# Kernel optimization log

Hardware: AMD Instinct MI355X
Metric: run time of the kernel (lower is better)

The kernel has to match this reference:

```python
import jax, jax.numpy as jnp
import numpy as np
import math

N_PTS = 262144
STEP_LENGTH = math.sqrt(3.0) / 1024.0  # step_length = sqrt(3)/steps


def pos_enc(x):
    # classic NeRF frequency encoding: identity + sin/cos at 10 octaves -> 3 + 3*2*10 = 63
    freqs = 2.0 ** jnp.arange(10, dtype=x.dtype)            # [10]
    xb = x[..., :, None] * freqs                            # [N,3,10]
    xb = xb.reshape(x.shape[0], -1)                         # [N,30]
    return jnp.concatenate([x, jnp.sin(xb), jnp.cos(xb)], axis=-1)  # [N,63]


def dir_enc(u):
    # 26-dim frequency encoding of (dir+1)/2 (color head input 283 = 256 + 26 + 1).
    # 13 sin/cos pairs: per-channel octaves 2^0..2^4, truncated to 13 frequencies.
    freqs = 2.0 ** jnp.arange(5, dtype=u.dtype)             # [5]
    z = (u[..., :, None] * freqs).reshape(u.shape[0], -1)[:, :13]  # [N,13]
    return jnp.concatenate([jnp.sin(z), jnp.cos(z)], axis=-1)      # [N,26]


def linear(x, w, b):
    return x @ w.T + b


def setup_inputs() -> dict:
    key = jax.random.key(0)
    ks = jax.random.split(key, 16)
    s = 0.05
    inp = {
        "position": jax.random.uniform(ks[0], (N_PTS, 3), dtype=jnp.float32),
        "direction": jax.random.uniform(ks[1], (N_PTS, 3), dtype=jnp.float32, minval=-1.0, maxval=1.0),
        "w1_in": jax.random.normal(ks[2], (256, 63), jnp.float32) * s,
        "b1_in": jnp.zeros((256,), jnp.float32),
        "w1_h": jax.random.normal(ks[3], (3, 256, 256), jnp.float32) * s,
        "b1_h": jnp.zeros((3, 256), jnp.float32),
        "w2_in": jax.random.normal(ks[4], (256, 319), jnp.float32) * s,
        "b2_in": jnp.zeros((256,), jnp.float32),
        "w2_h": jax.random.normal(ks[5], (3, 256, 256), jnp.float32) * s,
        "b2_h": jnp.zeros((3, 256), jnp.float32),
        # sigma head Linear(256,1)
        "w_sigma": jax.random.normal(ks[6], (1, 256), jnp.float32) * s,
        "b_sigma": jnp.zeros((1,), jnp.float32),
        # color head Linear(283,128) -> ReLU -> Linear(128,3)
        "w_c1": jax.random.normal(ks[7], (128, 283), jnp.float32) * s,
        "b_c1": jnp.zeros((128,), jnp.float32),
        "w_c2": jax.random.normal(ks[8], (3, 128), jnp.float32) * s,
        "b_c2": jnp.zeros((3,), jnp.float32),
    }
    return inp


def reference(position, direction,
              w1_in, b1_in, w1_h, b1_h,
              w2_in, b2_in, w2_h, b2_h,
              w_sigma, b_sigma, w_c1, b_c1, w_c2, b_c2):
    pe = pos_enc(position)                                  # [N,63]
    h = jax.nn.relu(linear(pe, w1_in, b1_in))               # [N,256]
    for i in range(3):
        h = jax.nn.relu(linear(h, w1_h[i], b1_h[i]))
    g = jax.nn.relu(linear(jnp.concatenate([h, pe], axis=-1), w2_in, b2_in))  # [N,256]
    for i in range(3):
        g = jax.nn.relu(linear(g, w2_h[i], b2_h[i]))
    sigma_raw = linear(g, w_sigma, b_sigma)                 # [N,1]
    # get_alpha: 1 - exp(-relu(sigma) * step_length)
    alphas = 1.0 - jnp.exp(-jax.nn.relu(sigma_raw) * STEP_LENGTH)             # [N,1]
    # get_rgb: shares base features; concat [256 | 26 | 1] = 283
    de = dir_enc((direction + 1.0) * 0.5)                   # [N,26]
    feats = jnp.concatenate([g, de, sigma_raw], axis=-1)    # [N,283]
    rgb = jax.nn.sigmoid(linear(jax.nn.relu(linear(feats, w_c1, b_c1)), w_c2, b_c2))  # [N,3]
    return (rgb, alphas)
```

## Files before the change

### kernel.cpp

```cpp
#include <hip/hip_runtime.h>
#include <hip/hip_bf16.h>

#define N_PTS 262144
#define STEP_LEN 0.0016914558667664818f

using f32x4 = __attribute__((ext_vector_type(4))) float;
using s8 = __attribute__((ext_vector_type(8))) short;

__device__ __forceinline__ float bf2f(short s) {
    union { unsigned int u; float f; } v;
    v.u = ((unsigned int)(unsigned short)s) << 16;
    return v.f;
}
__device__ __forceinline__ short f2bf(float f) {
    __hip_bfloat16 h = __float2bfloat16(f);
    return *reinterpret_cast<short*>(&h);
}

#define OFF_W1    0
#define OFF_L1H0  16384
#define OFF_L1H1  81920
#define OFF_L1H2  147456
#define OFF_W2    212992
#define OFF_L2H0  294912
#define OFF_L2H1  360448
#define OFF_L2H2  425984
#define OFF_C1G   491520
#define OFF_C1DE  524288
#define OFF_WSIG  528384
#define OFF_WC2   528640
#define WS_ELEMS  529024

__device__ __forceinline__ float hid_val(const float* __restrict__ W, int e) {
    int j = e & 7, lane = (e >> 3) & 63, nt = (e >> 9) & 15, ks = e >> 13;
    int n = nt * 16 + (lane & 15), hi = lane >> 4;
    int f = ks * 32 + ((j >> 2) << 4) + hi * 4 + (j & 3);
    return W[n * 256 + f];
}

__global__ void prep_weights(const float* __restrict__ w1_in,
                             const float* __restrict__ w1_h,
                             const float* __restrict__ w2_in,
                             const float* __restrict__ w2_h,
                             const float* __restrict__ w_c1,
                             const float* __restrict__ w_sigma,
                             const float* __restrict__ w_c2,
                             __hip_bfloat16* __restrict__ ws) {
    int i = blockIdx.x * blockDim.x + threadIdx.x;
    if (i >= WS_ELEMS) return;
    float v;
    if (i < OFF_L1H0) {
        int e = i;
        int j = e & 7, lane = (e >> 3) & 63, nt = (e >> 9) & 15, ks = e >> 13;
        int n = nt * 16 + (lane & 15), hi = lane >> 4;
        int f = ks * 32 + hi * 8 + j;
        v = (f < 63) ? w1_in[n * 63 + f] : 0.f;
    } else if (i < OFF_W2) {
        int e = i - OFF_L1H0; int sub = e >> 16; e &= 65535;
        v = hid_val(w1_h + sub * 65536, e);
    } else if (i < OFF_L2H0) {
        int e = i - OFF_W2;
        int j = e & 7, lane = (e >> 3) & 63, nt = (e >> 9) & 15, ks = e >> 13;
        int n = nt * 16 + (lane & 15), hi = lane >> 4;
        if (ks < 8) {
            int f = ks * 32 + ((j >> 2) << 4) + hi * 4 + (j & 3);
            v = w2_in[n * 319 + f];
        } else {
            int pf = (ks - 8) * 32 + hi * 8 + j;
            v = (pf < 63) ? w2_in[n * 319 + 256 + pf] : 0.f;
        }
    } else if (i < OFF_C1G) {
        int e = i - OFF_L2H0; int sub = e >> 16; e &= 65535;
        v = hid_val(w2_h + sub * 65536, e);
    } else if (i < OFF_C1DE) {
        int e = i - OFF_C1G;
        int j = e & 7, lane = (e >> 3) & 63, nt = (e >> 9) & 7, ks = e >> 12;
        int n = nt * 16 + (lane & 15), hi = lane >> 4;
        int f = ks * 32 + ((j >> 2) << 4) + hi * 4 + (j & 3);
        v = w_c1[n * 283 + f];
    } else if (i < OFF_WSIG) {
        int e = i - OFF_C1DE;
        int j = e & 7, lane = (e >> 3) & 63, nt = (e >> 9) & 7;
        int n = nt * 16 + (lane & 15), hi = lane >> 4;
        int k = 256 + hi * 8 + j;
        v = (k < 283) ? w_c1[n * 283 + k] : 0.f;
    } else if (i < OFF_WC2) {
        int e = i - OFF_WSIG;
        int j = e & 7, hi = (e >> 3) & 3, ks = e >> 5;
        int f = ks * 32 + ((j >> 2) << 4) + hi * 4 + (j & 3);
        v = w_sigma[f];
    } else {
        int e = i - OFF_WC2;
        int j = e & 7, hi = (e >> 3) & 3, ks = (e >> 5) & 3, ch = e >> 7;
        int f = ks * 32 + ((j >> 2) << 4) + hi * 4 + (j & 3);
        v = w_c2[ch * 128 + f];
    }
    ws[i] = __float2bfloat16(v);
}

__device__ __forceinline__ float enc3(int f, float x0, float x1, float x2) {
    if (f < 3) return (f == 0) ? x0 : ((f == 1) ? x1 : x2);
    if (f < 33) {
        int q = f - 3; int c = q / 10, o = q % 10;
        float xc = (c == 0) ? x0 : ((c == 1) ? x1 : x2);
        return __sinf(xc * (float)(1 << o));
    }
    if (f < 63) {
        int q = f - 33; int c = q / 10, o = q % 10;
        float xc = (c == 0) ? x0 : ((c == 1) ? x1 : x2);
        return __cosf(xc * (float)(1 << o));
    }
    return 0.f;
}

#define MFMA16 __builtin_amdgcn_mfma_f32_16x16x32_bf16

#define CHUNK1(WB, KSL, FA, FB) do { \
    _Pragma("unroll") \
    for (int nt = 0; nt < 16; ++nt) { \
        const s8 w = *(const s8*)((WB) + (((KSL)*16 + nt)*64 + lane)*16); \
        acc[nt][0] = MFMA16(w, (FA), acc[nt][0], 0, 0, 0); \
        acc[nt][1] = MFMA16(w, (FB), acc[nt][1], 0, 0, 0); \
    } } while (0)

#define CHUNK2(WB, KB) do { \
    _Pragma("unroll") \
    for (int ksl = 0; ksl < 2; ++ksl) { \
        _Pragma("unroll") \
        for (int nt = 0; nt < 16; ++nt) { \
            const s8 w = *(const s8*)((WB) + ((ksl*16 + nt)*64 + lane)*16); \
            acc[nt][0] = MFMA16(w, actA[(KB) + ksl], acc[nt][0], 0, 0, 0); \
            acc[nt][1] = MFMA16(w, actB[(KB) + ksl], acc[nt][1], 0, 0, 0); \
        } } } while (0)

#define CHUNKC4(WB, KB) do { \
    _Pragma("unroll") \
    for (int ksl = 0; ksl < 4; ++ksl) { \
        _Pragma("unroll") \
        for (int nt = 0; nt < 8; ++nt) { \
            const s8 w = *(const s8*)((WB) + ((ksl*8 + nt)*64 + lane)*16); \
            acc[nt][0] = MFMA16(w, actA[(KB) + ksl], acc[nt][0], 0, 0, 0); \
            acc[nt][1] = MFMA16(w, actB[(KB) + ksl], acc[nt][1], 0, 0, 0); \
        } } } while (0)

#define CHUNKCDE(WB) do { \
    _Pragma("unroll") \
    for (int nt = 0; nt < 8; ++nt) { \
        const s8 w = *(const s8*)((WB) + (nt*64 + lane)*16); \
        acc[nt][0] = MFMA16(w, deA, acc[nt][0], 0, 0, 0); \
        acc[nt][1] = MFMA16(w, deB, acc[nt][1], 0, 0, 0); \
    } } while (0)

#define CONVERT(BP) do { \
    _Pragma("unroll") \
    for (int nt = 0; nt < 16; ++nt) { \
        const f32x4 b4 = *(const f32x4*)((BP) + nt*16 + hi4); \
        _Pragma("unroll") \
        for (int r = 0; r < 4; ++r) { \
            actA[nt >> 1][((nt & 1) << 2) | r] = f2bf(fmaxf(acc[nt][0][r] + b4[r], 0.f)); \
            actB[nt >> 1][((nt & 1) << 2) | r] = f2bf(fmaxf(acc[nt][1][r] + b4[r], 0.f)); \
            acc[nt][0][r] = 0.f; acc[nt][1][r] = 0.f; \
        } } } while (0)

__global__ __launch_bounds__(256, 2) void nerf_fused(
    const float* __restrict__ pos, const float* __restrict__ dir,
    const __hip_bfloat16* __restrict__ ws,
    const float* __restrict__ b1_in, const float* __restrict__ b1_h,
    const float* __restrict__ b2_in, const float* __restrict__ b2_h,
    const float* __restrict__ b_sigma, const float* __restrict__ b_c1,
    const float* __restrict__ b_c2,
    float* __restrict__ out) {

    __shared__ __align__(16) char Lds[65536];
    char* const B0 = Lds;
    char* const B1 = Lds + 32768;

    const int t = threadIdx.x;
    const int lane = t & 63;
    const int wid = t >> 6;
    const int hi = lane >> 4;
    const int col = lane & 15;
    const int hi4 = hi * 4;
    const int row0 = blockIdx.x * 128;
    const int gA = row0 + wid * 32 + col;
    const int gB = gA + 16;
    const char* wsB = (const char*)ws;

    auto stageC = [&](int srcEl, char* dst, int bytes) {
        const char* src = wsB + (long)srcEl * 2;
        for (int rnd = 0; rnd < bytes; rnd += 4096) {
            int off = rnd + wid * 1024;
            __builtin_amdgcn_global_load_lds(
                (const unsigned int*)(src + off + lane * 16),
                (unsigned int*)(dst + off), 16, 0, 0);
        }
    };

    stageC(OFF_W1, B0, 32768);

    s8 peA0, peA1, peB0, peB1;
    {
        float xa0 = pos[gA*3], xa1 = pos[gA*3+1], xa2 = pos[gA*3+2];
        float xb0 = pos[gB*3], xb1 = pos[gB*3+1], xb2 = pos[gB*3+2];
#pragma unroll
        for (int j = 0; j < 8; ++j) {
            int f0 = hi * 8 + j, f1 = 32 + hi * 8 + j;
            peA0[j] = f2bf(enc3(f0, xa0, xa1, xa2));
            peA1[j] = f2bf(enc3(f1, xa0, xa1, xa2));
            peB0[j] = f2bf(enc3(f0, xb0, xb1, xb2));
            peB1[j] = f2bf(enc3(f1, xb0, xb1, xb2));
        }
    }

    f32x4 acc[16][2];
#pragma unroll
    for (int nt = 0; nt < 16; ++nt) { acc[nt][0] = f32x4{0,0,0,0}; acc[nt][1] = f32x4{0,0,0,0}; }
    s8 actA[8], actB[8];

    __syncthreads();
    stageC(1*16384, B1, 32768);
    CHUNK1(B0, 0, peA0, peB0); CHUNK1(B0, 1, peA1, peB1); CONVERT(b1_in);
    __syncthreads();
    stageC( 2*16384, B0, 32768); CHUNK2(B1, 0); __syncthreads();
    stageC( 3*16384, B1, 32768); CHUNK2(B0, 2); __syncthreads();
    stageC( 4*16384, B0, 32768); CHUNK2(B1, 4); __syncthreads();
    stageC( 5*16384, B1, 32768); CHUNK2(B0, 6); CONVERT(b1_h + 0);   __syncthreads();
    stageC( 6*16384, B0, 32768); CHUNK2(B1, 0); __syncthreads();
    stageC( 7*16384, B1, 32768); CHUNK2(B0, 2); __syncthreads();
    stageC( 8*16384, B0, 32768); CHUNK2(B1, 4); __syncthreads();
    stageC( 9*16384, B1, 32768); CHUNK2(B0, 6); CONVERT(b1_h + 256); __syncthreads();
    stageC(10*16384, B0, 32768); CHUNK2(B1, 0); __syncthreads();
    stageC(11*16384, B1, 32768); CHUNK2(B0, 2); __syncthreads();
    stageC(12*16384, B0, 32768); CHUNK2(B1, 4); __syncthreads();
    stageC(13*16384, B1, 32768); CHUNK2(B0, 6); CONVERT(b1_h + 512); __syncthreads();
    stageC(14*16384, B0, 32768); CHUNK2(B1, 0); __syncthreads();
    stageC(15*16384, B1, 32768); CHUNK2(B0, 2); __syncthreads();
    stageC(16*16384, B0, 32768); CHUNK2(B1, 4); __syncthreads();
    stageC(17*16384, B1, 32768); CHUNK2(B0, 6); __syncthreads();
    stageC(18*16384, B0, 32768);
    CHUNK1(B1, 0, peA0, peB0); CHUNK1(B1, 1, peA1, peB1); CONVERT(b2_in);
    __syncthreads();
    stageC(19*16384, B1, 32768); CHUNK2(B0, 0); __syncthreads();
    stageC(20*16384, B0, 32768); CHUNK2(B1, 2); __syncthreads();
    stageC(21*16384, B1, 32768); CHUNK2(B0, 4); __syncthreads();
    stageC(22*16384, B0, 32768); CHUNK2(B1, 6); CONVERT(b2_h + 0);   __syncthreads();
    stageC(23*16384, B1, 32768); CHUNK2(B0, 0); __syncthreads();
    stageC(24*16384, B0, 32768); CHUNK2(B1, 2); __syncthreads();
    stageC(25*16384, B1, 32768); CHUNK2(B0, 4); __syncthreads();
    stageC(26*16384, B0, 32768); CHUNK2(B1, 6); CONVERT(b2_h + 256); __syncthreads();
    stageC(27*16384, B1, 32768); CHUNK2(B0, 0); __syncthreads();
    stageC(28*16384, B0, 32768); CHUNK2(B1, 2); __syncthreads();
    stageC(29*16384, B1, 32768); CHUNK2(B0, 4); __syncthreads();
    stageC(OFF_C1G,  B0, 32768); CHUNK2(B1, 6); CONVERT(b2_h + 512); __syncthreads();

    stageC(OFF_C1G + 16384, B1, 32768);
    float srA, srB;
    {
        float sA = 0.f, sB = 0.f;
#pragma unroll
        for (int ks = 0; ks < 8; ++ks) {
            const s8 wv = *(const s8*)(wsB + (OFF_WSIG + ks * 32 + hi * 8) * 2);
#pragma unroll
            for (int j = 0; j < 8; ++j) {
                sA += bf2f(actA[ks][j]) * bf2f(wv[j]);
                sB += bf2f(actB[ks][j]) * bf2f(wv[j]);
            }
        }
        sA += __shfl_xor(sA, 16); sA += __shfl_xor(sA, 32);
        sB += __shfl_xor(sB, 16); sB += __shfl_xor(sB, 32);
        srA = sA + b_sigma[0]; srB = sB + b_sigma[0];
        if (hi == 0) {
            out[3 * N_PTS + gA] = 1.f - __expf(-fmaxf(srA, 0.f) * STEP_LEN);
            out[3 * N_PTS + gB] = 1.f - __expf(-fmaxf(srB, 0.f) * STEP_LEN);
        }
    }
    s8 deA, deB;
    {
        float uA0 = (dir[gA*3+0] + 1.f) * 0.5f;
        float uA1 = (dir[gA*3+1] + 1.f) * 0.5f;
        float uA2 = (dir[gA*3+2] + 1.f) * 0.5f;
        float uB0 = (dir[gB*3+0] + 1.f) * 0.5f;
        float uB1 = (dir[gB*3+1] + 1.f) * 0.5f;
        float uB2 = (dir[gB*3+2] + 1.f) * 0.5f;
#pragma unroll
        for (int j = 0; j < 8; ++j) {
            int d = hi * 8 + j;
            float vA, vB;
            if (d < 13) {
                int c = d / 5, o = d % 5; float s = (float)(1 << o);
                vA = __sinf(((c == 0) ? uA0 : (c == 1) ? uA1 : uA2) * s);
                vB = __sinf(((c == 0) ? uB0 : (c == 1) ? uB1 : uB2) * s);
            } else if (d < 26) {
                int q = d - 13; int c = q / 5, o = q % 5; float s = (float)(1 << o);
                vA = __cosf(((c == 0) ? uA0 : (c == 1) ? uA1 : uA2) * s);
                vB = __cosf(((c == 0) ? uB0 : (c == 1) ? uB1 : uB2) * s);
            } else if (d == 26) {
                vA = srA; vB = srB;
            } else {
                vA = 0.f; vB = 0.f;
            }
            deA[j] = f2bf(vA); deB[j] = f2bf(vB);
        }
    }
    CHUNKC4(B0, 0);
    __syncthreads();

    stageC(OFF_C1DE, B0, 8192);
    CHUNKC4(B1, 4);
    __syncthreads();

    CHUNKCDE(B0);
    s8 c1A[4], c1B[4];
#pragma unroll
    for (int nt = 0; nt < 8; ++nt) {
        const f32x4 b4 = *(const f32x4*)(b_c1 + nt * 16 + hi4);
#pragma unroll
        for (int r = 0; r < 4; ++r) {
            c1A[nt >> 1][((nt & 1) << 2) | r] = f2bf(fmaxf(acc[nt][0][r] + b4[r], 0.f));
            c1B[nt >> 1][((nt & 1) << 2) | r] = f2bf(fmaxf(acc[nt][1][r] + b4[r], 0.f));
        }
    }
#pragma unroll
    for (int ch = 0; ch < 3; ++ch) {
        float rA = 0.f, rB = 0.f;
#pragma unroll
        for (int ks = 0; ks < 4; ++ks) {
            const s8 wv = *(const s8*)(wsB + (OFF_WC2 + (ch * 4 + ks) * 32 + hi * 8) * 2);
#pragma unroll
            for (int j = 0; j < 8; ++j) {
                rA += bf2f(c1A[ks][j]) * bf2f(wv[j]);
                rB += bf2f(c1B[ks][j]) * bf2f(wv[j]);
            }
        }
        rA += __shfl_xor(rA, 16); rA += __shfl_xor(rA, 32);
        rB += __shfl_xor(rB, 16); rB += __shfl_xor(rB, 32);
        if (hi == 0) {
            out[gA * 3 + ch] = 1.f / (1.f + __expf(-(rA + b_c2[ch])));
            out[gB * 3 + ch] = 1.f / (1.f + __expf(-(rB + b_c2[ch])));
        }
    }
}

extern "C" void kernel_launch(void* const* d_in, const int* in_sizes, int n_in,
                              void* d_out, int out_size, void* d_ws, size_t ws_size,
                              hipStream_t stream) {
    const float* position = (const float*)d_in[0];
    const float* direction = (const float*)d_in[1];
    const float* w1_in = (const float*)d_in[2];
    const float* b1_in = (const float*)d_in[3];
    const float* w1_h  = (const float*)d_in[4];
    const float* b1_h  = (const float*)d_in[5];
    const float* w2_in = (const float*)d_in[6];
    const float* b2_in = (const float*)d_in[7];
    const float* w2_h  = (const float*)d_in[8];
    const float* b2_h  = (const float*)d_in[9];
    const float* w_sigma = (const float*)d_in[10];
    const float* b_sigma = (const float*)d_in[11];
    const float* w_c1  = (const float*)d_in[12];
    const float* b_c1  = (const float*)d_in[13];
    const float* w_c2  = (const float*)d_in[14];
    const float* b_c2  = (const float*)d_in[15];
    float* out = (float*)d_out;
    __hip_bfloat16* ws = (__hip_bfloat16*)d_ws;

    prep_weights<<<(WS_ELEMS + 255) / 256, 256, 0, stream>>>(
        w1_in, w1_h, w2_in, w2_h, w_c1, w_sigma, w_c2, ws);

    nerf_fused<<<N_PTS / 128, 256, 0, stream>>>(
        position, direction, ws,
        b1_in, b1_h, b2_in, b2_h,
        b_sigma, b_c1, b_c2, out);
}
```

Measured before the change: 269.5 us.

## Read MFMA weight fragments directly from global memory instead of LDS double-buffering

Removes the 64KB LDS double-buffer and the global_load_lds staging pipeline with its many __syncthreads. Each lane now loads its bf16 weight fragments straight from global memory (relying on L1/L2 caching of the roughly 1.3MB shared weights), and hidden layers become a rolled loop with plain s_barrier calls. Freeing LDS could allow more resident blocks, but every wave now issues its own global loads for weights that were previously shared through LDS, so MFMA throughput depends on cache latency and bandwidth. Accumulator zeroing is folded into the first MFMA of each layer.

```diff
diff --git a/kernel.cpp b/kernel.cpp
--- a/kernel.cpp
+++ b/kernel.cpp
@@ -115,42 +115,6 @@
 
 #define MFMA16 __builtin_amdgcn_mfma_f32_16x16x32_bf16
 
-#define CHUNK1(WB, KSL, FA, FB) do { \
-    _Pragma("unroll") \
-    for (int nt = 0; nt < 16; ++nt) { \
-        const s8 w = *(const s8*)((WB) + (((KSL)*16 + nt)*64 + lane)*16); \
-        acc[nt][0] = MFMA16(w, (FA), acc[nt][0], 0, 0, 0); \
-        acc[nt][1] = MFMA16(w, (FB), acc[nt][1], 0, 0, 0); \
-    } } while (0)
-
-#define CHUNK2(WB, KB) do { \
-    _Pragma("unroll") \
-    for (int ksl = 0; ksl < 2; ++ksl) { \
-        _Pragma("unroll") \
-        for (int nt = 0; nt < 16; ++nt) { \
-            const s8 w = *(const s8*)((WB) + ((ksl*16 + nt)*64 + lane)*16); \
-            acc[nt][0] = MFMA16(w, actA[(KB) + ksl], acc[nt][0], 0, 0, 0); \
-            acc[nt][1] = MFMA16(w, actB[(KB) + ksl], acc[nt][1], 0, 0, 0); \
-        } } } while (0)
-
-#define CHUNKC4(WB, KB) do { \
-    _Pragma("unroll") \
-    for (int ksl = 0; ksl < 4; ++ksl) { \
-        _Pragma("unroll") \
-        for (int nt = 0; nt < 8; ++nt) { \
-            const s8 w = *(const s8*)((WB) + ((ksl*8 + nt)*64 + lane)*16); \
-            acc[nt][0] = MFMA16(w, actA[(KB) + ksl], acc[nt][0], 0, 0, 0); \
-            acc[nt][1] = MFMA16(w, actB[(KB) + ksl], acc[nt][1], 0, 0, 0); \
-        } } } while (0)
-
-#define CHUNKCDE(WB) do { \
-    _Pragma("unroll") \
-    for (int nt = 0; nt < 8; ++nt) { \
-        const s8 w = *(const s8*)((WB) + (nt*64 + lane)*16); \
-        acc[nt][0] = MFMA16(w, deA, acc[nt][0], 0, 0, 0); \
-        acc[nt][1] = MFMA16(w, deB, acc[nt][1], 0, 0, 0); \
-    } } while (0)
-
 #define CONVERT(BP) do { \
     _Pragma("unroll") \
     for (int nt = 0; nt < 16; ++nt) { \
@@ -159,8 +123,20 @@
         for (int r = 0; r < 4; ++r) { \
             actA[nt >> 1][((nt & 1) << 2) | r] = f2bf(fmaxf(acc[nt][0][r] + b4[r], 0.f)); \
             actB[nt >> 1][((nt & 1) << 2) | r] = f2bf(fmaxf(acc[nt][1][r] + b4[r], 0.f)); \
-            acc[nt][0][r] = 0.f; acc[nt][1][r] = 0.f; \
         } } } while (0)
+
+#define HLAYER(WB, BP) do { \
+    _Pragma("unroll") \
+    for (int ks = 0; ks < 8; ++ks) { \
+        _Pragma("unroll") \
+        for (int nt = 0; nt < 16; ++nt) { \
+            const s8 w = *(const s8*)((WB) + (ks * 16 + nt) * 1024); \
+            acc[nt][0] = MFMA16(w, actA[ks], ks ? acc[nt][0] : Z, 0, 0, 0); \
+            acc[nt][1] = MFMA16(w, actB[ks], ks ? acc[nt][1] : Z, 0, 0, 0); \
+        } } \
+    CONVERT(BP); \
+    __builtin_amdgcn_s_barrier(); \
+} while (0)
 
 __global__ __launch_bounds__(256, 2) void nerf_fused(
     const float* __restrict__ pos, const float* __restrict__ dir,
@@ -170,10 +146,6 @@
     const float* __restrict__ b_sigma, const float* __restrict__ b_c1,
     const float* __restrict__ b_c2,
     float* __restrict__ out) {
-
-    __shared__ __align__(16) char Lds[65536];
-    char* const B0 = Lds;
-    char* const B1 = Lds + 32768;
 
     const int t = threadIdx.x;
     const int lane = t & 63;
@@ -185,18 +157,7 @@
     const int gA = row0 + wid * 32 + col;
     const int gB = gA + 16;
     const char* wsB = (const char*)ws;
-
-    auto stageC = [&](int srcEl, char* dst, int bytes) {
-        const char* src = wsB + (long)srcEl * 2;
-        for (int rnd = 0; rnd < bytes; rnd += 4096) {
-            int off = rnd + wid * 1024;
-            __builtin_amdgcn_global_load_lds(
-                (const unsigned int*)(src + off + lane * 16),
-                (unsigned int*)(dst + off), 16, 0, 0);
-        }
-    };
-
-    stageC(OFF_W1, B0, 32768);
+    const char* wlane = wsB + lane * 16;
 
     s8 peA0, peA1, peB0, peB1;
     {
@@ -213,47 +174,57 @@
     }
 
     f32x4 acc[16][2];
-#pragma unroll
-    for (int nt = 0; nt < 16; ++nt) { acc[nt][0] = f32x4{0,0,0,0}; acc[nt][1] = f32x4{0,0,0,0}; }
     s8 actA[8], actB[8];
-
-    __syncthreads();
-    stageC(1*16384, B1, 32768);
-    CHUNK1(B0, 0, peA0, peB0); CHUNK1(B0, 1, peA1, peB1); CONVERT(b1_in);
-    __syncthreads();
-    stageC( 2*16384, B0, 32768); CHUNK2(B1, 0); __syncthreads();
-    stageC( 3*16384, B1, 32768); CHUNK2(B0, 2); __syncthreads();
-    stageC( 4*16384, B0, 32768); CHUNK2(B1, 4); __syncthreads();
-    stageC( 5*16384, B1, 32768); CHUNK2(B0, 6); CONVERT(b1_h + 0);   __syncthreads();
-    stageC( 6*16384, B0, 32768); CHUNK2(B1, 0); __syncthreads();
-    stageC( 7*16384, B1, 32768); CHUNK2(B0, 2); __syncthreads();
-    stageC( 8*16384, B0, 32768); CHUNK2(B1, 4); __syncthreads();
-    stageC( 9*16384, B1, 32768); CHUNK2(B0, 6); CONVERT(b1_h + 256); __syncthreads();
-    stageC(10*16384, B0, 32768); CHUNK2(B1, 0); __syncthreads();
-    stageC(11*16384, B1, 32768); CHUNK2(B0, 2); __syncthreads();
-    stageC(12*16384, B0, 32768); CHUNK2(B1, 4); __syncthreads();
-    stageC(13*16384, B1, 32768); CHUNK2(B0, 6); CONVERT(b1_h + 512); __syncthreads();
-    stageC(14*16384, B0, 32768); CHUNK2(B1, 0); __syncthreads();
-    stageC(15*16384, B1, 32768); CHUNK2(B0, 2); __syncthreads();
-    stageC(16*16384, B0, 32768); CHUNK2(B1, 4); __syncthreads();
-    stageC(17*16384, B1, 32768); CHUNK2(B0, 6); __syncthreads();
-    stageC(18*16384, B0, 32768);
-    CHUNK1(B1, 0, peA0, peB0); CHUNK1(B1, 1, peA1, peB1); CONVERT(b2_in);
-    __syncthreads();
-    stageC(19*16384, B1, 32768); CHUNK2(B0, 0); __syncthreads();
-    stageC(20*16384, B0, 32768); CHUNK2(B1, 2); __syncthreads();
-    stageC(21*16384, B1, 32768); CHUNK2(B0, 4); __syncthreads();
-    stageC(22*16384, B0, 32768); CHUNK2(B1, 6); CONVERT(b2_h + 0);   __syncthreads();
-    stageC(23*16384, B1, 32768); CHUNK2(B0, 0); __syncthreads();
-    stageC(24*16384, B0, 32768); CHUNK2(B1, 2); __syncthreads();
-    stageC(25*16384, B1, 32768); CHUNK2(B0, 4); __syncthreads();
-    stageC(26*16384, B0, 32768); CHUNK2(B1, 6); CONVERT(b2_h + 256); __syncthreads();
-    stageC(27*16384, B1, 32768); CHUNK2(B0, 0); __syncthreads();
-    stageC(28*16384, B0, 32768); CHUNK2(B1, 2); __syncthreads();
-    stageC(29*16384, B1, 32768); CHUNK2(B0, 4); __syncthreads();
-    stageC(OFF_C1G,  B0, 32768); CHUNK2(B1, 6); CONVERT(b2_h + 512); __syncthreads();
-
-    stageC(OFF_C1G + 16384, B1, 32768);
+    const f32x4 Z = {0.f, 0.f, 0.f, 0.f};
+
+#pragma unroll
+    for (int nt = 0; nt < 16; ++nt) {
+        const s8 w0 = *(const s8*)(wlane + (long)OFF_W1 * 2 + (0 * 16 + nt) * 1024);
+        const s8 w1 = *(const s8*)(wlane + (long)OFF_W1 * 2 + (1 * 16 + nt) * 1024);
+        acc[nt][0] = MFMA16(w0, peA0, Z, 0, 0, 0);
+        acc[nt][0] = MFMA16(w1, peA1, acc[nt][0], 0, 0, 0);
+        acc[nt][1] = MFMA16(w0, peB0, Z, 0, 0, 0);
+        acc[nt][1] = MFMA16(w1, peB1, acc[nt][1], 0, 0, 0);
+    }
+    CONVERT(b1_in);
+    __builtin_amdgcn_s_barrier();
+
+#pragma unroll 1
+    for (int l = 0; l < 3; ++l) {
+        const char* wb = wlane + (long)(OFF_L1H0 + l * 65536) * 2;
+        HLAYER(wb, b1_h + l * 256);
+    }
+
+    {
+        const char* wb = wlane + (long)OFF_W2 * 2;
+#pragma unroll
+        for (int ks = 0; ks < 8; ++ks) {
+#pragma unroll
+            for (int nt = 0; nt < 16; ++nt) {
+                const s8 w = *(const s8*)(wb + (ks * 16 + nt) * 1024);
+                acc[nt][0] = MFMA16(w, actA[ks], ks ? acc[nt][0] : Z, 0, 0, 0);
+                acc[nt][1] = MFMA16(w, actB[ks], ks ? acc[nt][1] : Z, 0, 0, 0);
+            }
+        }
+#pragma unroll
+        for (int nt = 0; nt < 16; ++nt) {
+            const s8 w8 = *(const s8*)(wb + (8 * 16 + nt) * 1024);
+            const s8 w9 = *(const s8*)(wb + (9 * 16 + nt) * 1024);
+            acc[nt][0] = MFMA16(w8, peA0, acc[nt][0], 0, 0, 0);
+            acc[nt][0] = MFMA16(w9, peA1, acc[nt][0], 0, 0, 0);
+            acc[nt][1] = MFMA16(w8, peB0, acc[nt][1], 0, 0, 0);
+            acc[nt][1] = MFMA16(w9, peB1, acc[nt][1], 0, 0, 0);
+        }
+        CONVERT(b2_in);
+        __builtin_amdgcn_s_barrier();
+    }
+
+#pragma unroll 1
+    for (int l = 0; l < 3; ++l) {
+        const char* wb = wlane + (long)(OFF_L2H0 + l * 65536) * 2;
+        HLAYER(wb, b2_h + l * 256);
+    }
+
     float srA, srB;
     {
         float sA = 0.f, sB = 0.f;
@@ -274,6 +245,7 @@
             out[3 * N_PTS + gB] = 1.f - __expf(-fmaxf(srB, 0.f) * STEP_LEN);
         }
     }
+
     s8 deA, deB;
     {
         float uA0 = (dir[gA*3+0] + 1.f) * 0.5f;
@@ -302,14 +274,26 @@
             deA[j] = f2bf(vA); deB[j] = f2bf(vB);
         }
     }
-    CHUNKC4(B0, 0);
-    __syncthreads();
-
-    stageC(OFF_C1DE, B0, 8192);
-    CHUNKC4(B1, 4);
-    __syncthreads();
-
-    CHUNKCDE(B0);
+
+    {
+        const char* wb = wlane + (long)OFF_C1G * 2;
+#pragma unroll
+        for (int ks = 0; ks < 8; ++ks) {
+#pragma unroll
+            for (int nt = 0; nt < 8; ++nt) {
+                const s8 w = *(const s8*)(wb + (ks * 8 + nt) * 1024);
+                acc[nt][0] = MFMA16(w, actA[ks], ks ? acc[nt][0] : Z, 0, 0, 0);
+                acc[nt][1] = MFMA16(w, actB[ks], ks ? acc[nt][1] : Z, 0, 0, 0);
+            }
+        }
+        const char* wd = wlane + (long)OFF_C1DE * 2;
+#pragma unroll
+        for (int nt = 0; nt < 8; ++nt) {
+            const s8 w = *(const s8*)(wd + nt * 1024);
+            acc[nt][0] = MFMA16(w, deA, acc[nt][0], 0, 0, 0);
+            acc[nt][1] = MFMA16(w, deB, acc[nt][1], 0, 0, 0);
+        }
+    }
     s8 c1A[4], c1B[4];
 #pragma unroll
     for (int nt = 0; nt < 8; ++nt) {
@@ -320,6 +304,7 @@
             c1B[nt >> 1][((nt & 1) << 2) | r] = f2bf(fmaxf(acc[nt][1][r] + b4[r], 0.f));
         }
     }
+
 #pragma unroll
     for (int ch = 0; ch < 3; ++ch) {
         float rA = 0.f, rB = 0.f;
```

After: 565.4 us. 110% more time.
